# Optimization experiments

Measured on AMD Instinct MI355X. Metric: run time of the kernel, lower is better.

## Reference

```python
import jax, jax.numpy as jnp
import numpy as np

B, A_IN, C_IN, H, W_ = 8, 16, 4, 64, 64   # batch, input atoms, input capsules, spatial
K, C_OUT, A_OUT, ROUTINGS = 5, 8, 32, 3
EPS = 1e-7


def setup_inputs() -> dict:
    key = jax.random.key(0)
    k1, k2 = jax.random.split(key)
    x = jax.random.normal(k1, (B, A_IN, C_IN, H, W_), dtype=jnp.float32)
    # kaiming_uniform_(fan_in, relu): bound = sqrt(3) * sqrt(2) / sqrt(fan_in)
    fan_in = A_IN * K * K
    bound = float(np.sqrt(6.0 / fan_in))
    W = jax.random.uniform(k2, (C_OUT * A_OUT, A_IN, K, K), jnp.float32, -bound, bound)
    b = jnp.full((1, 1, C_OUT, A_OUT), 0.1, dtype=jnp.float32)
    return {"x": x, "W": W, "b": b}


def _squash(v):
    # v: (..., atoms); SegCaps squash with epsilon inside sqrt
    sq = jnp.sum(v * v, axis=-1, keepdims=True)
    return v * (sq / (1.0 + sq) / jnp.sqrt(sq + EPS))


def reference(x, W, b):
    # Faithful to torch: permute then raw row-major reshapes (byte reinterpret)
    t = jnp.transpose(x, (2, 0, 3, 4, 1))                      # (C_IN, B, H, W, A_IN)
    t = t.reshape(C_IN * B, H, W_, A_IN).reshape(-1, A_IN, H, W_)
    conv = jax.lax.conv_general_dilated(
        t, W, window_strides=(1, 1), padding="SAME",
        dimension_numbers=("NCHW", "OIHW", "NCHW"))             # (C_IN*B, C_OUT*A_OUT, h, w)
    ch, cw = conv.shape[2], conv.shape[3]
    votes = conv.reshape(B, C_IN, ch, cw, C_OUT, A_OUT)         # raw reinterpret, as in torch
    biases = jnp.tile(b, (ch, cw, 1, 1))                        # (h, w, C_OUT, A_OUT)

    # dynamic routing (SegCaps update_routing)
    logits = jnp.zeros((B, C_IN, ch, cw, C_OUT), dtype=votes.dtype)
    activation = None
    for _ in range(ROUTINGS):
        route = jax.nn.softmax(logits, axis=-1)                 # (B, Cin, h, w, Cout)
        preact = jnp.einsum("bihwo,bihwoa->bhwoa", route, votes) + biases
        activation = _squash(preact)                            # (B, h, w, Cout, A)
        agreement = jnp.einsum("bihwoa,bhwoa->bihwo", votes, activation)
        logits = logits + agreement
    return jnp.transpose(activation, (0, 4, 3, 1, 2))           # (B, A_OUT, C_OUT, h, w)
```

## Files before the change

### kernel.cpp

```cpp
#include <hip/hip_runtime.h>
#include <hip/hip_bf16.h>


typedef _Float16 half8 __attribute__((ext_vector_type(8)));
typedef _Float16 half4v __attribute__((ext_vector_type(4)));
typedef float floatx4 __attribute__((ext_vector_type(4)));

#define EPSF 1e-7f

__global__ __launch_bounds__(256) void k_pack2(const float* __restrict__ x,
                                               _Float16* __restrict__ th) {
  __shared__ float lin[32 * 306 + 18];
  const int bid = blockIdx.x;
  const int n   = bid >> 3;
  const int a0h = (bid >> 2) & 1;
  const int W0  = (bid & 3) * 16;
  const int ci = n >> 3, b0 = n & 7;
  const int tid = threadIdx.x;
  const float* xb = x + b0 * 262144 + ci * 4096 + W0;

  for (int p = 0; p < 8; ++p) {
    int rr = p * 64 + (tid >> 2);
    int q  = (tid & 3) * 4;
    int a1 = rr >> 5, m = rr & 31;
    float4 v = *(const float4*)(xb + a1 * 16384 + (a0h * 32 + m) * 64 + q);
    float* d = lin + m * 306 + a1 * 18 + q;
    d[0] = v.x; d[1] = v.y; d[2] = v.z; d[3] = v.w;
  }
  __syncthreads();

  _Float16* tb = th + (size_t)n * 65536 + a0h * 32768 + W0 * 128;
  for (int hh = 0; hh < 4; ++hh) {
    int w1 = tid >> 4, a1 = tid & 15;
    half8 v;
#pragma unroll
    for (int j = 0; j < 8; ++j)
      v[j] = (_Float16)lin[(j * 4 + hh) * 306 + a1 * 18 + w1];
    *(half8*)(tb + hh * 8192 + w1 * 128 + a1 * 8) = v;
  }
}

__global__ __launch_bounds__(256) void k_packw(const float* __restrict__ W,
                                               _Float16* __restrict__ Wp) {
  int id = blockIdx.x * 256 + threadIdx.x;
  int a  = id & 15;
  int oc = (id >> 4) & 255;
  int kk = id >> 12;
  Wp[id] = (kk < 25) ? (_Float16)W[oc * 400 + a * 25 + kk] : (_Float16)0.0f;
}

__global__ __launch_bounds__(256) void k_conv(const _Float16* __restrict__ th,
                                              const _Float16* __restrict__ Wp,
                                              _Float16* __restrict__ votes) {
  __shared__ _Float16 lds[5440];
  const int y = blockIdx.x;
  const int n = blockIdx.y;
  const int tid = threadIdx.x;

  for (int c = tid; c < 680; c += 256) {
    int a0h = c / 340;
    int rem = c - a0h * 340;
    int r   = rem / 68;
    int col = rem - r * 68;
    int row = y + r - 2;
    half8 v = {};
    if (col >= 2 && col <= 65 && row >= 0 && row < 64)
      v = *(const half8*)(th + (size_t)(((n * 2 + a0h) * 64 + row) * 64 + (col - 2)) * 8);
    *(half8*)(lds + c * 8) = v;
  }
  __syncthreads();

  const int lane  = tid & 63;
  const int wv    = tid >> 6;
  const int col16 = lane & 15;
  const int quad  = lane >> 4;
  const int t     = quad >> 1;
  const int a0h   = quad & 1;
  const int m0    = wv * 64;

  floatx4 acc[4][4] = {};

  const _Float16* wbase = Wp + (size_t)t * 4096 + (m0 + col16) * 16 + a0h * 8;
  half8 af[4], an[4], bf[4];
#pragma unroll
  for (int oct = 0; oct < 4; ++oct)
    af[oct] = *(const half8*)(wbase + oct * 256);

  for (int s = 0; s < 13; ++s) {
    int kkb = 2 * s + t; if (kkb > 24) kkb = 24;
    int ky = kkb / 5;
    int kx = kkb - ky * 5;
    const _Float16* lb = lds + (a0h * 340 + ky * 68 + col16 + kx) * 8;
#pragma unroll
    for (int xt = 0; xt < 4; ++xt)
      bf[xt] = *(const half8*)(lb + xt * 128);
    int sn = (s + 1 < 13) ? (s + 1) : s;
#pragma unroll
    for (int oct = 0; oct < 4; ++oct)
      an[oct] = *(const half8*)(wbase + (size_t)sn * 8192 + oct * 256);
#pragma unroll
    for (int oct = 0; oct < 4; ++oct)
#pragma unroll
      for (int xt = 0; xt < 4; ++xt)
        acc[oct][xt] = __builtin_amdgcn_mfma_f32_16x16x32_f16(
            af[oct], bf[xt], acc[oct][xt], 0, 0, 0);
#pragma unroll
    for (int oct = 0; oct < 4; ++oct) af[oct] = an[oct];
  }

  _Float16* vbase = votes + (size_t)n * 1048576 + y * 64;
#pragma unroll
  for (int oct = 0; oct < 4; ++oct)
#pragma unroll
    for (int xt = 0; xt < 4; ++xt)
#pragma unroll
      for (int r = 0; r < 4; ++r) {
        int oc = m0 + oct * 16 + quad * 4 + r;
        int xx = xt * 16 + col16;
        vbase[(size_t)oc * 4096 + xx] = (_Float16)acc[oct][xt][r];
      }
}

__global__ __launch_bounds__(256) void k_routing2(
    const _Float16* __restrict__ votes, const float* __restrict__ bias,
    float* __restrict__ out) {
  __shared__ float so[256 * 36];
  const int tid  = threadIdx.x;
  const int lane = tid & 63;
  const int wv   = tid >> 6;
  const int bid  = blockIdx.x;
  const int bv = bid >> 7;
  const int h  = (bid >> 1) & 63;
  const int W0 = (bid & 1) * 32;

  float4 bia = *(const float4*)(bias + lane * 4);
  const int o  = lane >> 3;
  const int a0 = (lane & 7) * 4;

  for (int k = 0; k < 8; ++k) {
    const int wl = wv * 8 + k;
    const int w  = W0 + wl;
    const _Float16* vb = votes + (size_t)bv * 4194304 + h * 16384 + w * 256 + lane * 4;
    float4 v[4];
#pragma unroll
    for (int i = 0; i < 4; ++i) {
      half4v hv = *(const half4v*)(vb + (size_t)i * 1048576);
      v[i] = make_float4((float)hv.x, (float)hv.y, (float)hv.z, (float)hv.w);
    }

    float logit[4] = {0.f, 0.f, 0.f, 0.f};
    float act[4];

#pragma unroll
    for (int r = 0; r < 3; ++r) {
      float route[4];
#pragma unroll
      for (int i = 0; i < 4; ++i) {
        float m = logit[i];
        m = fmaxf(m, __shfl_xor(m, 8, 64));
        m = fmaxf(m, __shfl_xor(m, 16, 64));
        m = fmaxf(m, __shfl_xor(m, 32, 64));
        float e = __expf(logit[i] - m);
        float s = e;
        s += __shfl_xor(s, 8, 64);
        s += __shfl_xor(s, 16, 64);
        s += __shfl_xor(s, 32, 64);
        route[i] = e / s;
      }
      float pr[4] = {bia.x, bia.y, bia.z, bia.w};
#pragma unroll
      for (int i = 0; i < 4; ++i) {
        pr[0] = fmaf(route[i], v[i].x, pr[0]);
        pr[1] = fmaf(route[i], v[i].y, pr[1]);
        pr[2] = fmaf(route[i], v[i].z, pr[2]);
        pr[3] = fmaf(route[i], v[i].w, pr[3]);
      }
      float sq = pr[0]*pr[0] + pr[1]*pr[1] + pr[2]*pr[2] + pr[3]*pr[3];
      sq += __shfl_xor(sq, 1, 64);
      sq += __shfl_xor(sq, 2, 64);
      sq += __shfl_xor(sq, 4, 64);
      float scale = sq / (1.f + sq) / sqrtf(sq + EPSF);
#pragma unroll
      for (int j = 0; j < 4; ++j) act[j] = pr[j] * scale;

      if (r < 2) {
#pragma unroll
        for (int i = 0; i < 4; ++i) {
          float ag = v[i].x*act[0] + v[i].y*act[1] + v[i].z*act[2] + v[i].w*act[3];
          ag += __shfl_xor(ag, 1, 64);
          ag += __shfl_xor(ag, 2, 64);
          ag += __shfl_xor(ag, 4, 64);
          logit[i] += ag;
        }
      }
    }

#pragma unroll
    for (int j = 0; j < 4; ++j)
      so[((a0 + j) * 8 + o) * 36 + wl] = act[j];
  }
  __syncthreads();

  float* ob = out + (size_t)bv * 1048576 + h * 64 + W0;
  for (int p = 0; p < 8; ++p) {
    int r  = p * 32 + (tid >> 3);
    int w0 = (tid & 7) * 4;
    float4 v = *(const float4*)(so + r * 36 + w0);
    *(float4*)(ob + (size_t)r * 4096 + w0) = v;
  }
}

extern "C" void kernel_launch(void* const* d_in, const int* in_sizes, int n_in,
                              void* d_out, int out_size, void* d_ws, size_t ws_size,
                              hipStream_t stream) {
  const float* x  = (const float*)d_in[0];
  const float* W  = (const float*)d_in[1];
  const float* b  = (const float*)d_in[2];
  float* out = (float*)d_out;

  _Float16* th    = (_Float16*)d_ws;
  _Float16* Wp    = th + 2097152;
  _Float16* votes = Wp + 106496;

  k_pack2<<<256, 256, 0, stream>>>(x, th);
  k_packw<<<416, 256, 0, stream>>>(W, Wp);
  k_conv<<<dim3(64, 32), 256, 0, stream>>>(th, Wp, votes);
  k_routing2<<<1024, 256, 0, stream>>>(votes, b, out);
}
```

Before: 142.3 us.

## Fuse conv and dynamic routing into one kernel, merge input/weight packing

Merges the input and weight packing kernels into one launch and fuses the MFMA convolution with the routing step. Each block computes the conv tile for four input images into LDS and gathers the votes into registers, so the fp16 votes tensor never goes to global memory. Routing then writes its output directly with scalar strided stores instead of staging through LDS. This removes a large global write and read of votes plus two launches, but each conv slab is now reloaded per image, register pressure rises, and the output stores are less coalesced.

```diff
diff --git a/kernel.cpp b/kernel.cpp
--- a/kernel.cpp
+++ b/kernel.cpp
@@ -8,149 +8,152 @@
 
 #define EPSF 1e-7f
 
-__global__ __launch_bounds__(256) void k_pack2(const float* __restrict__ x,
-                                               _Float16* __restrict__ th) {
-  __shared__ float lin[32 * 306 + 18];
-  const int bid = blockIdx.x;
-  const int n   = bid >> 3;
-  const int a0h = (bid >> 2) & 1;
-  const int W0  = (bid & 3) * 16;
-  const int ci = n >> 3, b0 = n & 7;
+__global__ __launch_bounds__(256) void k_prep(const float* __restrict__ x,
+                                              const float* __restrict__ W,
+                                              _Float16* __restrict__ th,
+                                              _Float16* __restrict__ Wp) {
   const int tid = threadIdx.x;
-  const float* xb = x + b0 * 262144 + ci * 4096 + W0;
-
-  for (int p = 0; p < 8; ++p) {
-    int rr = p * 64 + (tid >> 2);
-    int q  = (tid & 3) * 4;
-    int a1 = rr >> 5, m = rr & 31;
-    float4 v = *(const float4*)(xb + a1 * 16384 + (a0h * 32 + m) * 64 + q);
-    float* d = lin + m * 306 + a1 * 18 + q;
-    d[0] = v.x; d[1] = v.y; d[2] = v.z; d[3] = v.w;
-  }
-  __syncthreads();
-
-  _Float16* tb = th + (size_t)n * 65536 + a0h * 32768 + W0 * 128;
-  for (int hh = 0; hh < 4; ++hh) {
-    int w1 = tid >> 4, a1 = tid & 15;
-    half8 v;
-#pragma unroll
-    for (int j = 0; j < 8; ++j)
-      v[j] = (_Float16)lin[(j * 4 + hh) * 306 + a1 * 18 + w1];
-    *(half8*)(tb + hh * 8192 + w1 * 128 + a1 * 8) = v;
+  if (blockIdx.x < 256) {
+    __shared__ float lin[32 * 306 + 18];
+    const int bid = blockIdx.x;
+    const int n   = bid >> 3;
+    const int a0h = (bid >> 2) & 1;
+    const int W0  = (bid & 3) * 16;
+    const int ci = n >> 3, b0 = n & 7;
+    const float* xb = x + b0 * 262144 + ci * 4096 + W0;
+    for (int p = 0; p < 8; ++p) {
+      int rr = p * 64 + (tid >> 2);
+      int qq = (tid & 3) * 4;
+      int a1 = rr >> 5, m = rr & 31;
+      float4 v = *(const float4*)(xb + a1 * 16384 + (a0h * 32 + m) * 64 + qq);
+      float* d = lin + m * 306 + a1 * 18 + qq;
+      d[0] = v.x; d[1] = v.y; d[2] = v.z; d[3] = v.w;
+    }
+    __syncthreads();
+    _Float16* tb = th + (size_t)n * 65536 + a0h * 32768 + W0 * 128;
+    for (int hh = 0; hh < 4; ++hh) {
+      int w1 = tid >> 4, a1 = tid & 15;
+      half8 v;
+#pragma unroll
+      for (int j = 0; j < 8; ++j)
+        v[j] = (_Float16)lin[(j * 4 + hh) * 306 + a1 * 18 + w1];
+      *(half8*)(tb + hh * 8192 + w1 * 128 + a1 * 8) = v;
+    }
+  } else {
+    int id = (blockIdx.x - 256) * 256 + tid;
+    int a  = id & 15;
+    int oc = (id >> 4) & 255;
+    int kk = id >> 12;
+    Wp[id] = (kk < 25) ? (_Float16)W[oc * 400 + a * 25 + kk] : (_Float16)0.0f;
   }
 }
 
-__global__ __launch_bounds__(256) void k_packw(const float* __restrict__ W,
-                                               _Float16* __restrict__ Wp) {
-  int id = blockIdx.x * 256 + threadIdx.x;
-  int a  = id & 15;
-  int oc = (id >> 4) & 255;
-  int kk = id >> 12;
-  Wp[id] = (kk < 25) ? (_Float16)W[oc * 400 + a * 25 + kk] : (_Float16)0.0f;
-}
-
-__global__ __launch_bounds__(256) void k_conv(const _Float16* __restrict__ th,
-                                              const _Float16* __restrict__ Wp,
-                                              _Float16* __restrict__ votes) {
-  __shared__ _Float16 lds[5440];
-  const int y = blockIdx.x;
-  const int n = blockIdx.y;
-  const int tid = threadIdx.x;
-
-  for (int c = tid; c < 680; c += 256) {
-    int a0h = c / 340;
-    int rem = c - a0h * 340;
-    int r   = rem / 68;
-    int col = rem - r * 68;
-    int row = y + r - 2;
-    half8 v = {};
-    if (col >= 2 && col <= 65 && row >= 0 && row < 64)
-      v = *(const half8*)(th + (size_t)(((n * 2 + a0h) * 64 + row) * 64 + (col - 2)) * 8);
-    *(half8*)(lds + c * 8) = v;
-  }
-  __syncthreads();
-
-  const int lane  = tid & 63;
-  const int wv    = tid >> 6;
+__global__ __launch_bounds__(512, 2) void k_fused(
+    const _Float16* __restrict__ th, const _Float16* __restrict__ Wp,
+    const float* __restrict__ bias, float* __restrict__ out) {
+  __shared__ _Float16 vlds[16384];
+  __shared__ _Float16 slab[8704];
+  const int yq = blockIdx.x;
+  const int q  = blockIdx.y;
+  const int bv = blockIdx.z;
+  const int tid  = threadIdx.x;
+  const int lane = tid & 63;
+  const int wv   = tid >> 6;
+  const int yl4   = wv >> 1;
+  const int xh    = wv & 1;
   const int col16 = lane & 15;
   const int quad  = lane >> 4;
   const int t     = quad >> 1;
   const int a0h   = quad & 1;
-  const int m0    = wv * 64;
-
-  floatx4 acc[4][4] = {};
-
-  const _Float16* wbase = Wp + (size_t)t * 4096 + (m0 + col16) * 16 + a0h * 8;
-  half8 af[4], an[4], bf[4];
-#pragma unroll
-  for (int oct = 0; oct < 4; ++oct)
-    af[oct] = *(const half8*)(wbase + oct * 256);
-
-  for (int s = 0; s < 13; ++s) {
-    int kkb = 2 * s + t; if (kkb > 24) kkb = 24;
-    int ky = kkb / 5;
-    int kx = kkb - ky * 5;
-    const _Float16* lb = lds + (a0h * 340 + ky * 68 + col16 + kx) * 8;
-#pragma unroll
-    for (int xt = 0; xt < 4; ++xt)
-      bf[xt] = *(const half8*)(lb + xt * 128);
-    int sn = (s + 1 < 13) ? (s + 1) : s;
+
+  const _Float16* wbase = Wp + (size_t)t * 4096 + (q * 64 + col16) * 16 + a0h * 8;
+
+  half4v vfrag[4][8];
+
+#pragma unroll
+  for (int p = 0; p < 4; ++p) {
+    const int n = bv * 4 + p;
+    for (int c = tid; c < 1088; c += 512) {
+      int ah  = c / 544;
+      int rem = c - ah * 544;
+      int rr  = rem / 68;
+      int cc  = rem - rr * 68;
+      int row = yq * 4 + rr - 2;
+      int col = cc - 2;
+      half8 v = {};
+      if (row >= 0 && row < 64 && col >= 0 && col < 64)
+        v = *(const half8*)(th + (size_t)(((n * 2 + ah) * 64 + row) * 64 + col) * 8);
+      *(half8*)(slab + c * 8) = v;
+    }
+    __syncthreads();
+
+    floatx4 acc[4][2] = {};
+    half8 af[4], an[4], bf2[2];
 #pragma unroll
     for (int oct = 0; oct < 4; ++oct)
-      an[oct] = *(const half8*)(wbase + (size_t)sn * 8192 + oct * 256);
+      af[oct] = *(const half8*)(wbase + oct * 256);
+
+    for (int s = 0; s < 13; ++s) {
+      int kkb = 2 * s + t; if (kkb > 24) kkb = 24;
+      int ky = kkb / 5, kx = kkb - ky * 5;
+      const _Float16* lb = slab + (a0h * 4352 + (yl4 + ky) * 544
+                                   + (xh * 32 + col16 + kx) * 8);
+      bf2[0] = *(const half8*)(lb);
+      bf2[1] = *(const half8*)(lb + 128);
+      int sn = (s + 1 < 13) ? s + 1 : s;
+#pragma unroll
+      for (int oct = 0; oct < 4; ++oct)
+        an[oct] = *(const half8*)(wbase + (size_t)sn * 8192 + oct * 256);
+#pragma unroll
+      for (int oct = 0; oct < 4; ++oct)
+#pragma unroll
+        for (int xt = 0; xt < 2; ++xt)
+          acc[oct][xt] = __builtin_amdgcn_mfma_f32_16x16x32_f16(
+              af[oct], bf2[xt], acc[oct][xt], 0, 0, 0);
+#pragma unroll
+      for (int oct = 0; oct < 4; ++oct) af[oct] = an[oct];
+    }
+
 #pragma unroll
     for (int oct = 0; oct < 4; ++oct)
 #pragma unroll
-      for (int xt = 0; xt < 4; ++xt)
-        acc[oct][xt] = __builtin_amdgcn_mfma_f32_16x16x32_f16(
-            af[oct], bf[xt], acc[oct][xt], 0, 0, 0);
-#pragma unroll
-    for (int oct = 0; oct < 4; ++oct) af[oct] = an[oct];
+      for (int xt = 0; xt < 2; ++xt)
+#pragma unroll
+        for (int r = 0; r < 4; ++r) {
+          int ocl = oct * 16 + quad * 4 + r;
+          int xx  = (xh * 32 + xt * 16 + col16) ^ (quad << 4);
+          vlds[ocl * 256 + yl4 * 64 + xx] = (_Float16)acc[oct][xt][r];
+        }
+    __syncthreads();
+
+#pragma unroll
+    for (int k = 0; k < 8; ++k) {
+      int ocl = wv * 8 + k;
+      int xr  = ((lane * 4) & 63) ^ (((ocl >> 2) & 3) << 4);
+      vfrag[p][k] = *(const half4v*)(vlds + ocl * 256 + (lane >> 4) * 64 + xr);
+    }
+    __syncthreads();
   }
-
-  _Float16* vbase = votes + (size_t)n * 1048576 + y * 64;
-#pragma unroll
-  for (int oct = 0; oct < 4; ++oct)
-#pragma unroll
-    for (int xt = 0; xt < 4; ++xt)
-#pragma unroll
-      for (int r = 0; r < 4; ++r) {
-        int oc = m0 + oct * 16 + quad * 4 + r;
-        int xx = xt * 16 + col16;
-        vbase[(size_t)oc * 4096 + xx] = (_Float16)acc[oct][xt][r];
-      }
-}
-
-__global__ __launch_bounds__(256) void k_routing2(
-    const _Float16* __restrict__ votes, const float* __restrict__ bias,
-    float* __restrict__ out) {
-  __shared__ float so[256 * 36];
-  const int tid  = threadIdx.x;
-  const int lane = tid & 63;
-  const int wv   = tid >> 6;
-  const int bid  = blockIdx.x;
-  const int bv = bid >> 7;
-  const int h  = (bid >> 1) & 63;
-  const int W0 = (bid & 1) * 32;
 
   float4 bia = *(const float4*)(bias + lane * 4);
   const int o  = lane >> 3;
   const int a0 = (lane & 7) * 4;
 
+#pragma unroll
   for (int k = 0; k < 8; ++k) {
-    const int wl = wv * 8 + k;
-    const int w  = W0 + wl;
-    const _Float16* vb = votes + (size_t)bv * 4194304 + h * 16384 + w * 256 + lane * 4;
+    const int ocl = wv * 8 + k;
+    const int h = 16 * q + (ocl >> 2);
+    const int w = ((ocl & 3) << 4) | yq;
+
     float4 v[4];
 #pragma unroll
     for (int i = 0; i < 4; ++i) {
-      half4v hv = *(const half4v*)(vb + (size_t)i * 1048576);
+      half4v hv = vfrag[i][k];
       v[i] = make_float4((float)hv.x, (float)hv.y, (float)hv.z, (float)hv.w);
     }
 
     float logit[4] = {0.f, 0.f, 0.f, 0.f};
     float act[4];
-
 #pragma unroll
     for (int r = 0; r < 3; ++r) {
       float route[4];
@@ -195,18 +198,11 @@
       }
     }
 
+    float* ob = out + (size_t)bv * 1048576 + (size_t)a0 * 32768
+                    + o * 4096 + h * 64 + w;
 #pragma unroll
     for (int j = 0; j < 4; ++j)
-      so[((a0 + j) * 8 + o) * 36 + wl] = act[j];
-  }
-  __syncthreads();
-
-  float* ob = out + (size_t)bv * 1048576 + h * 64 + W0;
-  for (int p = 0; p < 8; ++p) {
-    int r  = p * 32 + (tid >> 3);
-    int w0 = (tid & 7) * 4;
-    float4 v = *(const float4*)(so + r * 36 + w0);
-    *(float4*)(ob + (size_t)r * 4096 + w0) = v;
+      ob[(size_t)j * 32768] = act[j];
   }
 }
 
@@ -218,12 +214,9 @@
   const float* b  = (const float*)d_in[2];
   float* out = (float*)d_out;
 
-  _Float16* th    = (_Float16*)d_ws;
-  _Float16* Wp    = th + 2097152;
-  _Float16* votes = Wp + 106496;
-
-  k_pack2<<<256, 256, 0, stream>>>(x, th);
-  k_packw<<<416, 256, 0, stream>>>(W, Wp);
-  k_conv<<<dim3(64, 32), 256, 0, stream>>>(th, Wp, votes);
-  k_routing2<<<1024, 256, 0, stream>>>(votes, b, out);
+  _Float16* th = (_Float16*)d_ws;
+  _Float16* Wp = th + 2097152;
+
+  k_prep<<<672, 256, 0, stream>>>(x, W, th, Wp);
+  k_fused<<<dim3(16, 4, 8), 512, 0, stream>>>(th, Wp, b, out);
 }
```

Result: slower. 246.1 us (+73.0%).

## Compute two output rows per conv block and merge pack kernels

Applied to the files above, without the earlier changes.

The conv kernel now computes two output rows per block, loading a 6-row input slab into LDS. Each weight fragment loaded from global memory feeds twice as many MFMAs, which halves weight traffic and block count. Separately, the input-pack and weight-pack kernels are merged into one launch to save launch overhead. The cost is double the accumulator registers (128 floats), which may lower occupancy, and the grid is smaller (1024 blocks).

```diff
diff --git a/kernel.cpp b/kernel.cpp
--- a/kernel.cpp
+++ b/kernel.cpp
@@ -8,65 +8,66 @@
 
 #define EPSF 1e-7f
 
-__global__ __launch_bounds__(256) void k_pack2(const float* __restrict__ x,
-                                               _Float16* __restrict__ th) {
-  __shared__ float lin[32 * 306 + 18];
-  const int bid = blockIdx.x;
-  const int n   = bid >> 3;
-  const int a0h = (bid >> 2) & 1;
-  const int W0  = (bid & 3) * 16;
-  const int ci = n >> 3, b0 = n & 7;
+__global__ __launch_bounds__(256) void k_prep(const float* __restrict__ x,
+                                              const float* __restrict__ W,
+                                              _Float16* __restrict__ th,
+                                              _Float16* __restrict__ Wp) {
   const int tid = threadIdx.x;
-  const float* xb = x + b0 * 262144 + ci * 4096 + W0;
-
-  for (int p = 0; p < 8; ++p) {
-    int rr = p * 64 + (tid >> 2);
-    int q  = (tid & 3) * 4;
-    int a1 = rr >> 5, m = rr & 31;
-    float4 v = *(const float4*)(xb + a1 * 16384 + (a0h * 32 + m) * 64 + q);
-    float* d = lin + m * 306 + a1 * 18 + q;
-    d[0] = v.x; d[1] = v.y; d[2] = v.z; d[3] = v.w;
-  }
-  __syncthreads();
-
-  _Float16* tb = th + (size_t)n * 65536 + a0h * 32768 + W0 * 128;
-  for (int hh = 0; hh < 4; ++hh) {
-    int w1 = tid >> 4, a1 = tid & 15;
-    half8 v;
-#pragma unroll
-    for (int j = 0; j < 8; ++j)
-      v[j] = (_Float16)lin[(j * 4 + hh) * 306 + a1 * 18 + w1];
-    *(half8*)(tb + hh * 8192 + w1 * 128 + a1 * 8) = v;
-  }
-}
-
-__global__ __launch_bounds__(256) void k_packw(const float* __restrict__ W,
-                                               _Float16* __restrict__ Wp) {
-  int id = blockIdx.x * 256 + threadIdx.x;
-  int a  = id & 15;
-  int oc = (id >> 4) & 255;
-  int kk = id >> 12;
-  Wp[id] = (kk < 25) ? (_Float16)W[oc * 400 + a * 25 + kk] : (_Float16)0.0f;
+  if (blockIdx.x < 256) {
+    __shared__ float lin[32 * 306 + 18];
+    const int bid = blockIdx.x;
+    const int n   = bid >> 3;
+    const int a0h = (bid >> 2) & 1;
+    const int W0  = (bid & 3) * 16;
+    const int ci = n >> 3, b0 = n & 7;
+    const float* xb = x + b0 * 262144 + ci * 4096 + W0;
+    for (int p = 0; p < 8; ++p) {
+      int rr = p * 64 + (tid >> 2);
+      int qq = (tid & 3) * 4;
+      int a1 = rr >> 5, m = rr & 31;
+      float4 v = *(const float4*)(xb + a1 * 16384 + (a0h * 32 + m) * 64 + qq);
+      float* d = lin + m * 306 + a1 * 18 + qq;
+      d[0] = v.x; d[1] = v.y; d[2] = v.z; d[3] = v.w;
+    }
+    __syncthreads();
+    _Float16* tb = th + (size_t)n * 65536 + a0h * 32768 + W0 * 128;
+    for (int hh = 0; hh < 4; ++hh) {
+      int w1 = tid >> 4, a1 = tid & 15;
+      half8 v;
+#pragma unroll
+      for (int j = 0; j < 8; ++j)
+        v[j] = (_Float16)lin[(j * 4 + hh) * 306 + a1 * 18 + w1];
+      *(half8*)(tb + hh * 8192 + w1 * 128 + a1 * 8) = v;
+    }
+  } else {
+    int id = (blockIdx.x - 256) * 256 + tid;
+    int a  = id & 15;
+    int oc = (id >> 4) & 255;
+    int kk = id >> 12;
+    Wp[id] = (kk < 25) ? (_Float16)W[oc * 400 + a * 25 + kk] : (_Float16)0.0f;
+  }
 }
 
 __global__ __launch_bounds__(256) void k_conv(const _Float16* __restrict__ th,
                                               const _Float16* __restrict__ Wp,
                                               _Float16* __restrict__ votes) {
-  __shared__ _Float16 lds[5440];
-  const int y = blockIdx.x;
-  const int n = blockIdx.y;
+  __shared__ _Float16 slab[6528];
+  const int y2 = blockIdx.x;
+  const int n  = blockIdx.y;
+  const int y0 = y2 * 2;
   const int tid = threadIdx.x;
 
-  for (int c = tid; c < 680; c += 256) {
-    int a0h = c / 340;
-    int rem = c - a0h * 340;
-    int r   = rem / 68;
-    int col = rem - r * 68;
-    int row = y + r - 2;
+  for (int c = tid; c < 816; c += 256) {
+    int ah  = c / 408;
+    int rem = c - ah * 408;
+    int rr  = rem / 68;
+    int cc  = rem - rr * 68;
+    int row = y0 + rr - 2;
+    int col = cc - 2;
     half8 v = {};
-    if (col >= 2 && col <= 65 && row >= 0 && row < 64)
-      v = *(const half8*)(th + (size_t)(((n * 2 + a0h) * 64 + row) * 64 + (col - 2)) * 8);
-    *(half8*)(lds + c * 8) = v;
+    if (row >= 0 && row < 64 && col >= 0 && col < 64)
+      v = *(const half8*)(th + (size_t)(((n * 2 + ah) * 64 + row) * 64 + col) * 8);
+    *(half8*)(slab + c * 8) = v;
   }
   __syncthreads();
 
@@ -78,10 +79,10 @@
   const int a0h   = quad & 1;
   const int m0    = wv * 64;
 
-  floatx4 acc[4][4] = {};
+  floatx4 acc[2][4][4] = {};
 
   const _Float16* wbase = Wp + (size_t)t * 4096 + (m0 + col16) * 16 + a0h * 8;
-  half8 af[4], an[4], bf[4];
+  half8 af[4], an[4];
 #pragma unroll
   for (int oct = 0; oct < 4; ++oct)
     af[oct] = *(const half8*)(wbase + oct * 256);
@@ -90,35 +91,43 @@
     int kkb = 2 * s + t; if (kkb > 24) kkb = 24;
     int ky = kkb / 5;
     int kx = kkb - ky * 5;
-    const _Float16* lb = lds + (a0h * 340 + ky * 68 + col16 + kx) * 8;
-#pragma unroll
-    for (int xt = 0; xt < 4; ++xt)
-      bf[xt] = *(const half8*)(lb + xt * 128);
-    int sn = (s + 1 < 13) ? (s + 1) : s;
+    const _Float16* lb = slab + a0h * 3264 + ky * 544 + (col16 + kx) * 8;
+    half8 bf[2][4];
+#pragma unroll
+    for (int yy = 0; yy < 2; ++yy)
+#pragma unroll
+      for (int xt = 0; xt < 4; ++xt)
+        bf[yy][xt] = *(const half8*)(lb + yy * 544 + xt * 128);
+    int sn = (s + 1 < 13) ? s + 1 : s;
 #pragma unroll
     for (int oct = 0; oct < 4; ++oct)
       an[oct] = *(const half8*)(wbase + (size_t)sn * 8192 + oct * 256);
 #pragma unroll
     for (int oct = 0; oct < 4; ++oct)
 #pragma unroll
+      for (int yy = 0; yy < 2; ++yy)
+#pragma unroll
+        for (int xt = 0; xt < 4; ++xt)
+          acc[yy][oct][xt] = __builtin_amdgcn_mfma_f32_16x16x32_f16(
+              af[oct], bf[yy][xt], acc[yy][oct][xt], 0, 0, 0);
+#pragma unroll
+    for (int oct = 0; oct < 4; ++oct) af[oct] = an[oct];
+  }
+
+#pragma unroll
+  for (int yy = 0; yy < 2; ++yy) {
+    _Float16* vbase = votes + (size_t)n * 1048576 + (y0 + yy) * 64;
+#pragma unroll
+    for (int oct = 0; oct < 4; ++oct)
+#pragma unroll
       for (int xt = 0; xt < 4; ++xt)
-        acc[oct][xt] = __builtin_amdgcn_mfma_f32_16x16x32_f16(
-            af[oct], bf[xt], acc[oct][xt], 0, 0, 0);
-#pragma unroll
-    for (int oct = 0; oct < 4; ++oct) af[oct] = an[oct];
-  }
-
-  _Float16* vbase = votes + (size_t)n * 1048576 + y * 64;
-#pragma unroll
-  for (int oct = 0; oct < 4; ++oct)
-#pragma unroll
-    for (int xt = 0; xt < 4; ++xt)
-#pragma unroll
-      for (int r = 0; r < 4; ++r) {
-        int oc = m0 + oct * 16 + quad * 4 + r;
-        int xx = xt * 16 + col16;
-        vbase[(size_t)oc * 4096 + xx] = (_Float16)acc[oct][xt][r];
-      }
+#pragma unroll
+        for (int r = 0; r < 4; ++r) {
+          int oc = m0 + oct * 16 + quad * 4 + r;
+          int xx = xt * 16 + col16;
+          vbase[(size_t)oc * 4096 + xx] = (_Float16)acc[yy][oct][xt][r];
+        }
+  }
 }
 
 __global__ __launch_bounds__(256) void k_routing2(
@@ -222,8 +231,7 @@
   _Float16* Wp    = th + 2097152;
   _Float16* votes = Wp + 106496;
 
-  k_pack2<<<256, 256, 0, stream>>>(x, th);
-  k_packw<<<416, 256, 0, stream>>>(W, Wp);
-  k_conv<<<dim3(64, 32), 256, 0, stream>>>(th, Wp, votes);
+  k_prep<<<672, 256, 0, stream>>>(x, W, th, Wp);
+  k_conv<<<dim3(32, 32), 256, 0, stream>>>(th, Wp, votes);
   k_routing2<<<1024, 256, 0, stream>>>(votes, b, out);
 }
```

Result: slower. 151.4 us (+6.4%).
